# Optimization experiments

Hardware: AMD Instinct MI355X
Metric: run time of the kernel (lower is better)

The kernel has to match this reference:

```python
import jax, jax.numpy as jnp
import numpy as np

N_NODES = 50000
N_EDGES = 1000000
D_IN = 128
HID = 64
N_GRAPHS = 256
NEG_SLOPE = 0.2


def _gatv2_layer(x, src, dst, Wl, Wr, att, b, n_nodes):
    # lin_l applied to source nodes, lin_r to target nodes (PyG GATv2Conv, heads=1)
    xl = x @ Wl.T  # [N, C]
    xr = x @ Wr.T  # [N, C]
    e = jax.nn.leaky_relu(xl[src] + xr[dst], NEG_SLOPE)  # [E, C]
    logits = e @ att  # [E]
    # segment softmax over destination node
    m = jax.ops.segment_max(logits, dst, num_segments=n_nodes)
    ex = jnp.exp(logits - m[dst])
    den = jax.ops.segment_sum(ex, dst, num_segments=n_nodes)
    alpha = ex / den[dst]  # [E]
    out = jax.ops.segment_sum(alpha[:, None] * xl[src], dst, num_segments=n_nodes)
    return out + b


def setup_inputs() -> dict:
    key = jax.random.key(0)
    ks = jax.random.split(key, 32)
    x = jax.random.normal(ks[0], (N_NODES, D_IN), dtype=jnp.float32)
    edge_index = jax.random.randint(ks[1], (2, N_EDGES), 0, N_NODES, dtype=jnp.int64)
    batch = jnp.sort(jax.random.randint(ks[2], (N_NODES,), 0, N_GRAPHS, dtype=jnp.int64))
    inp = {"x": x, "edge_index": edge_index, "batch": batch}
    dims = [D_IN, HID, HID]  # input dim per layer
    kidx = 3
    for i, din in enumerate(dims):
        inp[f"Wl{i}"] = jax.random.normal(ks[kidx], (HID, din), dtype=jnp.float32) * 0.1; kidx += 1
        inp[f"Wr{i}"] = jax.random.normal(ks[kidx], (HID, din), dtype=jnp.float32) * 0.1; kidx += 1
        inp[f"att{i}"] = jax.random.normal(ks[kidx], (HID,), dtype=jnp.float32) * 0.1; kidx += 1
        inp[f"b{i}"] = jnp.zeros((HID,), dtype=jnp.float32)
        inp[f"Rw{i}"] = jax.random.normal(ks[kidx], (HID, din), dtype=jnp.float32) * 0.1; kidx += 1
        inp[f"Rb{i}"] = jnp.zeros((HID,), dtype=jnp.float32)
    inp["Wf"] = jax.random.normal(ks[kidx], (1, HID), dtype=jnp.float32) * 0.1
    inp["bf"] = jnp.zeros((1,), dtype=jnp.float32)
    return inp


def reference(x, edge_index, batch, Wl0, Wr0, att0, b0, Rw0, Rb0,
              Wl1, Wr1, att1, b1, Rw1, Rb1,
              Wl2, Wr2, att2, b2, Rw2, Rb2, Wf, bf):
    n = x.shape[0]
    # add_self_loops=True (PyG default)
    loops = jnp.arange(n, dtype=edge_index.dtype)
    src = jnp.concatenate([edge_index[0], loops])
    dst = jnp.concatenate([edge_index[1], loops])
    layers = [(Wl0, Wr0, att0, b0, Rw0, Rb0),
              (Wl1, Wr1, att1, b1, Rw1, Rb1),
              (Wl2, Wr2, att2, b2, Rw2, Rb2)]
    for i, (Wl, Wr, att, b, Rw, Rb) in enumerate(layers):
        h = _gatv2_layer(x, src, dst, Wl, Wr, att, b, n) + (x @ Rw.T + Rb)  # res=True
        # norm=None -> Identity; dropout inactive at inference
        x = jax.nn.relu(h) if i < len(layers) - 1 else h
    # global_mean_pool
    sums = jax.ops.segment_sum(x, batch, num_segments=N_GRAPHS)
    cnt = jax.ops.segment_sum(jnp.ones((n,), x.dtype), batch, num_segments=N_GRAPHS)
    pooled = sums / jnp.maximum(cnt, 1.0)[:, None]
    return pooled @ Wf.T + bf
```

## Files before the change

### kernel.cpp

```cpp
#include <hip/hip_runtime.h>


#define NN 50000
#define NE 1000000
#define HID 64
#define DIN0 128
#define NG 256
#define NEG 0.2f

#define SCHUNK 1024
#define SNB ((NN + SCHUNK - 1) / SCHUNK)

typedef float f32x4 __attribute__((ext_vector_type(4)));
typedef short s8v __attribute__((ext_vector_type(8)));
typedef short s4v __attribute__((ext_vector_type(4)));
typedef __bf16 bf16x8 __attribute__((ext_vector_type(8)));
typedef _Float16 h2v __attribute__((ext_vector_type(2)));
typedef unsigned u32x2 __attribute__((ext_vector_type(2)));
typedef unsigned short u16;

__device__ __forceinline__ unsigned short f2bf(float f) {
    unsigned u = __float_as_uint(f);
    u = u + 0x7fffu + ((u >> 16) & 1u);
    return (unsigned short)(u >> 16);
}
__device__ __forceinline__ float bf2f(unsigned short v) {
    return __uint_as_float(((unsigned)v) << 16);
}
__device__ __forceinline__ short split_hi(float x) {
    return (short)f2bf(x);
}
__device__ __forceinline__ short split_lo(float x, short hi) {
    return (short)f2bf(x - bf2f((unsigned short)hi));
}
__device__ __forceinline__ h2v u2h(unsigned u) { return __builtin_bit_cast(h2v, u); }
__device__ __forceinline__ unsigned h2u(h2v h) { return __builtin_bit_cast(unsigned, h); }
__device__ __forceinline__ h2v pklo(unsigned a, unsigned b) {
    return u2h(__builtin_amdgcn_perm(b, a, 0x05040100u));
}
__device__ __forceinline__ h2v pkhi(unsigned a, unsigned b) {
    return u2h(__builtin_amdgcn_perm(b, a, 0x07060302u));
}
template <int CTRL>
__device__ __forceinline__ float dpp_mv(float v) {
    return __int_as_float(
        __builtin_amdgcn_update_dpp(0, __float_as_int(v), CTRL, 0xF, 0xF, true));
}
template <int OFF>
__device__ __forceinline__ float swz(float v) {
    return __int_as_float(__builtin_amdgcn_ds_swizzle(__float_as_int(v), OFF));
}
__device__ __forceinline__ float red32_add(float v) {
    unsigned u = __float_as_uint(v);
    u32x2 r = __builtin_amdgcn_permlane32_swap(u, u, false, false);
    return __uint_as_float(r[0]) + __uint_as_float(r[1]);
}
__device__ __forceinline__ float red32_max(float v) {
    unsigned u = __float_as_uint(v);
    u32x2 r = __builtin_amdgcn_permlane32_swap(u, u, false, false);
    return fmaxf(__uint_as_float(r[0]), __uint_as_float(r[1]));
}
__device__ __forceinline__ float octet_sum(float v) {
    v += dpp_mv<0xB1>(v);
    v += dpp_mv<0x4E>(v);
    v += swz<0x101F>(v);
    return v;
}
__device__ __forceinline__ float esum(float v) {
    v += dpp_mv<0x128>(v);
    v += swz<0x401F>(v);
    return red32_add(v);
}
__device__ __forceinline__ float emax(float v) {
    v = fmaxf(v, dpp_mv<0x128>(v));
    v = fmaxf(v, swz<0x401F>(v));
    return red32_max(v);
}

__global__ __launch_bounds__(256) void k_prep(
        const float* __restrict__ Wl0, const float* __restrict__ Wr0, const float* __restrict__ Rw0,
        const float* __restrict__ Wl1, const float* __restrict__ Wr1, const float* __restrict__ Rw1,
        const float* __restrict__ Wl2, const float* __restrict__ Wr2, const float* __restrict__ Rw2,
        const float* __restrict__ att0, const float* __restrict__ att1, const float* __restrict__ att2,
        short* __restrict__ Ws0, short* __restrict__ Ws1, short* __restrict__ Ws2,
        _Float16* __restrict__ attp,
        const int* __restrict__ batch,
        int* __restrict__ startg, int* __restrict__ endg,
        int* __restrict__ cnt8) {
    int i = blockIdx.x * 256 + threadIdx.x;
    if (i < 3 * HID) {
        int L = i >> 6, c = i & 63;
        const float* at = (L == 0) ? att0 : (L == 1) ? att1 : att2;
        float a = at[c];
        attp[L * 2 * HID + c] = (_Float16)(0.6f * a);
        attp[L * 2 * HID + HID + c] = (_Float16)(0.4f * a);
    }
    if (i < NN) {
#pragma unroll
        for (int g = 0; g < 8; g++) cnt8[g * NN + i] = 0;
        int g = batch[i];
        if (i == 0) {
            startg[g] = 0;
            for (int g2 = 0; g2 < g; g2++) { startg[g2] = 0; endg[g2] = 0; }
        } else if (batch[i - 1] != g) {
            startg[g] = i;
            for (int g2 = batch[i - 1] + 1; g2 < g; g2++) { startg[g2] = i; endg[g2] = i; }
        }
        if (i == NN - 1) {
            endg[g] = NN;
            for (int g2 = g + 1; g2 < NG; g2++) { startg[g2] = NN; endg[g2] = NN; }
        } else if (batch[i + 1] != g) {
            endg[g] = i + 1;
        }
    }
    const int L0N = 3 * HID * DIN0;
    const int L1N = 3 * HID * HID;
    if (i >= L0N + 2 * L1N) return;
    const float* Wm; short* Ws; int din, local;
    if (i < L0N) {
        local = i; din = DIN0; Ws = Ws0;
        int m = local / (DIN0 * HID);
        Wm = (m == 0) ? Wl0 : (m == 1) ? Wr0 : Rw0;
    } else if (i < L0N + L1N) {
        local = i - L0N; din = HID; Ws = Ws1;
        int m = local / (HID * HID);
        Wm = (m == 0) ? Wl1 : (m == 1) ? Wr1 : Rw1;
    } else {
        local = i - L0N - L1N; din = HID; Ws = Ws2;
        int m = local / (HID * HID);
        Wm = (m == 0) ? Wl2 : (m == 1) ? Wr2 : Rw2;
    }
    int m = local / (din * HID);
    int r = local - m * (din * HID);
    int c = r / din, k = r - c * din;
    float w = Wm[c * din + k];
    short hi = split_hi(w);
    short lo = split_lo(w, hi);
    Ws[(((m * 2 + 0) * HID + c) * din) + k] = hi;
    Ws[(((m * 2 + 1) * HID + c) * din) + k] = lo;
}

__global__ __launch_bounds__(256) void k_hist8(const int* __restrict__ edst,
                                               int* __restrict__ cnt8,
                                               u16* __restrict__ rank) {
    int* mycnt = cnt8 + (blockIdx.x & 7) * NN;
    for (int e = blockIdx.x * 256 + threadIdx.x; e < NE; e += 512 * 256) {
        int r = atomicAdd(&mycnt[edst[e]], 1);
        rank[e] = (u16)r;
    }
}

__global__ __launch_bounds__(256) void k_histscan(int* __restrict__ cnt8,
                                                  int* __restrict__ cnt,
                                                  int* __restrict__ part) {
    __shared__ int ws[4];
    int b = blockIdx.x, t = threadIdx.x;
    int i0 = b * SCHUNK + t * 4;
    int tot = 0;
#pragma unroll
    for (int j = 0; j < 4; j++) {
        int i = i0 + j;
        if (i < NN) {
            int s = 1;
#pragma unroll
            for (int g = 0; g < 8; g++) {
                int v = cnt8[g * NN + i];
                cnt8[g * NN + i] = s;
                s += v;
            }
            cnt[i] = s;
            tot += s;
        }
    }
#pragma unroll
    for (int o = 32; o; o >>= 1) tot += __shfl_xor(tot, o, 64);
    if ((t & 63) == 0) ws[t >> 6] = tot;
    __syncthreads();
    if (t == 0) part[b] = ws[0] + ws[1] + ws[2] + ws[3];
}

__global__ __launch_bounds__(256) void k_scan_emit(const int* __restrict__ cnt,
                                                   const int* __restrict__ part,
                                                   int* __restrict__ off,
                                                   u16* __restrict__ srcs) {
    __shared__ int tsum[256];
    __shared__ int baseSh;
    int b = blockIdx.x, t = threadIdx.x;
    if (t < 64) {
        int v = (t < b && t < SNB) ? part[t] : 0;
#pragma unroll
        for (int o = 32; o; o >>= 1) v += __shfl_xor(v, o, 64);
        if (t == 0) baseSh = v;
    }
    int i0 = b * SCHUNK + t * 4;
    int e[4], p[4];
    int s = 0;
#pragma unroll
    for (int j = 0; j < 4; j++) {
        int i = i0 + j;
        e[j] = (i < NN) ? cnt[i] : 0;
        p[j] = s;
        s += e[j];
    }
    tsum[t] = s;
    __syncthreads();
    for (int d = 1; d < 256; d <<= 1) {
        int v = (t >= d) ? tsum[t - d] : 0;
        __syncthreads();
        tsum[t] += v;
        __syncthreads();
    }
    int base = baseSh + ((t == 0) ? 0 : tsum[t - 1]);
#pragma unroll
    for (int j = 0; j < 4; j++) {
        int i = i0 + j;
        if (i < NN) {
            int v = base + p[j];
            off[i] = v;
            srcs[v] = (u16)i;
            if (i == NN - 1) off[NN] = v + e[j];
        }
    }
}

__global__ __launch_bounds__(256) void k_scatter_rank(
        const int* __restrict__ esrc, const int* __restrict__ edst,
        const int* __restrict__ off, const int* __restrict__ cnt8,
        const u16* __restrict__ rank, u16* __restrict__ srcs) {
    int e = blockIdx.x * 256 + threadIdx.x;
    if (e >= NE) return;
    int d = edst[e];
    int slice = (e >> 8) & 7;
    int pos = off[d] + cnt8[slice * NN + d] + (int)rank[e];
    srcs[pos] = (u16)esrc[e];
}

template <int DIN, bool RELU>
__global__ __launch_bounds__(256, 3) void k_gemm(
        const float* __restrict__ xin, const short* __restrict__ Ws,
        const float* __restrict__ bvec, const float* __restrict__ rb,
        _Float16* __restrict__ xl16, _Float16* __restrict__ xr16, float* __restrict__ acc) {
    constexpr int LROW = 40;
    __shared__ short lds[20480];
    short* xhi = lds;
    short* xlo = lds + 2560;

    const int tid = threadIdx.x;
    const int w = tid >> 6;
    const int lane = tid & 63;
    const int col = lane & 15;
    const int quad = lane >> 4;
    const int nb0 = blockIdx.x * 64;

    f32x4 d[3][4];
#pragma unroll
    for (int m = 0; m < 3; m++)
#pragma unroll
        for (int ct = 0; ct < 4; ct++) d[m][ct] = (f32x4){0.f, 0.f, 0.f, 0.f};

    for (int c0 = 0; c0 < DIN; c0 += 32) {
        if (c0) __syncthreads();
        for (int u = tid; u < 512; u += 256) {
            int row = u >> 3, kq = u & 7;
            int n = nb0 + row;
            float4 v = make_float4(0.f, 0.f, 0.f, 0.f);
            if (n < NN) {
                v = *(const float4*)&xin[(size_t)n * DIN + c0 + 4 * kq];
                if (RELU) {
                    v.x = fmaxf(v.x, 0.f); v.y = fmaxf(v.y, 0.f);
                    v.z = fmaxf(v.z, 0.f); v.w = fmaxf(v.w, 0.f);
                }
            }
            s4v h, l;
            short h0 = split_hi(v.x), l0 = split_lo(v.x, h0);
            short h1 = split_hi(v.y), l1 = split_lo(v.y, h1);
            short h2 = split_hi(v.z), l2 = split_lo(v.z, h2);
            short h3 = split_hi(v.w), l3 = split_lo(v.w, h3);
            h[0] = h0; h[1] = h1; h[2] = h2; h[3] = h3;
            l[0] = l0; l[1] = l1; l[2] = l2; l[3] = l3;
            *(s4v*)&xhi[row * LROW + 4 * kq] = h;
            *(s4v*)&xlo[row * LROW + 4 * kq] = l;
        }
        for (int u = tid; u < 1536; u += 256) {
            int mp = u >> 8;
            int r = u & 255;
            int c = r >> 2, q = r & 3;
            s8v v = *(const s8v*)&Ws[((mp * HID + c) * DIN) + c0 + 8 * q];
            *(s8v*)&lds[5120 + mp * 2560 + c * LROW + 8 * q] = v;
        }
        __syncthreads();

        bf16x8 a_h = __builtin_bit_cast(bf16x8,
            *(const s8v*)&xhi[(w * 16 + col) * LROW + quad * 8]);
        bf16x8 a_l = __builtin_bit_cast(bf16x8,
            *(const s8v*)&xlo[(w * 16 + col) * LROW + quad * 8]);

#pragma unroll
        for (int m = 0; m < 3; m++) {
#pragma unroll
            for (int ct = 0; ct < 4; ct++) {
                bf16x8 b_h = __builtin_bit_cast(bf16x8,
                    *(const s8v*)&lds[5120 + (m * 2 + 0) * 2560 + (ct * 16 + col) * LROW + quad * 8]);
                bf16x8 b_l = __builtin_bit_cast(bf16x8,
                    *(const s8v*)&lds[5120 + (m * 2 + 1) * 2560 + (ct * 16 + col) * LROW + quad * 8]);
                d[m][ct] = __builtin_amdgcn_mfma_f32_16x16x32_bf16(a_h, b_h, d[m][ct], 0, 0, 0);
                d[m][ct] = __builtin_amdgcn_mfma_f32_16x16x32_bf16(a_h, b_l, d[m][ct], 0, 0, 0);
                d[m][ct] = __builtin_amdgcn_mfma_f32_16x16x32_bf16(a_l, b_h, d[m][ct], 0, 0, 0);
            }
        }
    }

#pragma unroll
    for (int r = 0; r < 4; r++) {
        int n = nb0 + w * 16 + quad * 4 + r;
        if (n >= NN) continue;
        size_t base = (size_t)n * HID;
#pragma unroll
        for (int ct = 0; ct < 4; ct++) {
            int c = ct * 16 + col;
            xl16[base + c] = (_Float16)d[0][ct][r];
            xr16[base + c] = (_Float16)d[1][ct][r];
            acc[base + c] = d[2][ct][r] + bvec[c] + rb[c];
        }
    }
}

__global__ __launch_bounds__(256) void k_attn_dst(
        const int* __restrict__ off, const u16* __restrict__ srcs,
        const _Float16* __restrict__ xl16, const _Float16* __restrict__ xr16,
        const _Float16* __restrict__ attL, float* __restrict__ acc) {
    const int lane = threadIdx.x & 63;
    const int d = blockIdx.x * 4 + (threadIdx.x >> 6);
    if (d >= NN) return;
    const int e = lane >> 3;
    const int cg = lane & 7;

    const int lo = off[d], deg = off[d + 1] - lo;

    uint4 X = *(const uint4*)&xr16[(size_t)d * HID + 8 * cg];
    uint4 A6 = *(const uint4*)&attL[8 * cg];
    uint4 A4 = *(const uint4*)&attL[HID + 8 * cg];
    h2v xh0 = u2h(X.x), xh1 = u2h(X.y), xh2 = u2h(X.z), xh3 = u2h(X.w);
    h2v a60 = u2h(A6.x), a61 = u2h(A6.y), a62 = u2h(A6.z), a63 = u2h(A6.w);
    h2v a40 = u2h(A4.x), a41 = u2h(A4.y), a42 = u2h(A4.z), a43 = u2h(A4.w);

#define EDGE_DOT(S, U, PS)                                                     \
    {                                                                          \
        U = *(const uint4*)&xl16[(size_t)(S) * HID + 8 * cg];                  \
        h2v _v; unsigned _a; float _q0, _q1;                                   \
        _v = u2h(U.x) + xh0; _a = h2u(_v) & 0x7FFF7FFFu;                       \
        _q0 = __builtin_amdgcn_fdot2(a60, _v, 0.f, false);                     \
        _q1 = __builtin_amdgcn_fdot2(a40, u2h(_a), 0.f, false);                \
        _v = u2h(U.y) + xh1; _a = h2u(_v) & 0x7FFF7FFFu;                       \
        _q0 = __builtin_amdgcn_fdot2(a61, _v, _q0, false);                     \
        _q1 = __builtin_amdgcn_fdot2(a41, u2h(_a), _q1, false);                \
        _v = u2h(U.z) + xh2; _a = h2u(_v) & 0x7FFF7FFFu;                       \
        _q0 = __builtin_amdgcn_fdot2(a62, _v, _q0, false);                     \
        _q1 = __builtin_amdgcn_fdot2(a42, u2h(_a), _q1, false);                \
        _v = u2h(U.w) + xh3; _a = h2u(_v) & 0x7FFF7FFFu;                       \
        _q0 = __builtin_amdgcn_fdot2(a63, _v, _q0, false);                     \
        _q1 = __builtin_amdgcn_fdot2(a43, u2h(_a), _q1, false);                \
        PS = _q0 + _q1;                                                        \
    }

    float m = -INFINITY, l = 0.f;
    float4 oA = make_float4(0.f, 0.f, 0.f, 0.f);
    float4 oB = make_float4(0.f, 0.f, 0.f, 0.f);

    for (int base = 0; base < deg; base += 32) {
        const int rem = deg - base;
        int s0 = (int)srcs[lo + min(base + e, deg - 1)];
        int s1 = (int)srcs[lo + min(base + 8 + e, deg - 1)];
        int s2 = (int)srcs[lo + min(base + 16 + e, deg - 1)];
        int s3 = (int)srcs[lo + min(base + 24 + e, deg - 1)];

        uint4 U0, U1, U2, U3;
        float ps0, ps1, ps2, ps3;
        float t0, t1, t2 = -INFINITY, t3 = -INFINITY;
        EDGE_DOT(s0, U0, ps0);
        EDGE_DOT(s1, U1, ps1);
        t0 = octet_sum(ps0);
        t1 = octet_sum(ps1);
        if (base + e >= deg) t0 = -INFINITY;
        if (base + 8 + e >= deg) t1 = -INFINITY;

        const bool do2 = rem > 16;
        if (do2) {
            EDGE_DOT(s2, U2, ps2);
            t2 = octet_sum(ps2);
            if (base + 16 + e >= deg) t2 = -INFINITY;
            if (rem > 24) {
                EDGE_DOT(s3, U3, ps3);
                t3 = octet_sum(ps3);
                if (base + 24 + e >= deg) t3 = -INFINITY;
            } else {
                U3 = U0;
            }
        }

        float cm = emax(fmaxf(fmaxf(t0, t1), fmaxf(t2, t3)));
        if (cm > m) {
            float corr = __expf(m - cm);
            m = cm;
            l *= corr;
            oA.x *= corr; oA.y *= corr; oA.z *= corr; oA.w *= corr;
            oB.x *= corr; oB.y *= corr; oB.z *= corr; oB.w *= corr;
        }
        float p0 = __expf(t0 - m);
        float p1 = __expf(t1 - m);
        l += p0 + p1;
        h2v p01 = {(_Float16)p0, (_Float16)p1};
        oA.x = __builtin_amdgcn_fdot2(p01, pklo(U0.x, U1.x), oA.x, false);
        oA.y = __builtin_amdgcn_fdot2(p01, pkhi(U0.x, U1.x), oA.y, false);
        oA.z = __builtin_amdgcn_fdot2(p01, pklo(U0.y, U1.y), oA.z, false);
        oA.w = __builtin_amdgcn_fdot2(p01, pkhi(U0.y, U1.y), oA.w, false);
        oB.x = __builtin_amdgcn_fdot2(p01, pklo(U0.z, U1.z), oB.x, false);
        oB.y = __builtin_amdgcn_fdot2(p01, pkhi(U0.z, U1.z), oB.y, false);
        oB.z = __builtin_amdgcn_fdot2(p01, pklo(U0.w, U1.w), oB.z, false);
        oB.w = __builtin_amdgcn_fdot2(p01, pkhi(U0.w, U1.w), oB.w, false);
        if (do2) {
            float p2 = __expf(t2 - m);
            float p3 = __expf(t3 - m);
            l += p2 + p3;
            h2v p23 = {(_Float16)p2, (_Float16)p3};
            oA.x = __builtin_amdgcn_fdot2(p23, pklo(U2.x, U3.x), oA.x, false);
            oA.y = __builtin_amdgcn_fdot2(p23, pkhi(U2.x, U3.x), oA.y, false);
            oA.z = __builtin_amdgcn_fdot2(p23, pklo(U2.y, U3.y), oA.z, false);
            oA.w = __builtin_amdgcn_fdot2(p23, pkhi(U2.y, U3.y), oA.w, false);
            oB.x = __builtin_amdgcn_fdot2(p23, pklo(U2.z, U3.z), oB.x, false);
            oB.y = __builtin_amdgcn_fdot2(p23, pkhi(U2.z, U3.z), oB.y, false);
            oB.z = __builtin_amdgcn_fdot2(p23, pklo(U2.w, U3.w), oB.z, false);
            oB.w = __builtin_amdgcn_fdot2(p23, pkhi(U2.w, U3.w), oB.w, false);
        }
    }
#undef EDGE_DOT

    l    = esum(l);
    oA.x = esum(oA.x); oA.y = esum(oA.y);
    oA.z = esum(oA.z); oA.w = esum(oA.w);
    oB.x = esum(oB.x); oB.y = esum(oB.y);
    oB.z = esum(oB.z); oB.w = esum(oB.w);

    if (e == 0) {
        float inv = 1.f / l;
        float4* a4 = (float4*)&acc[(size_t)d * HID + 8 * cg];
        float4 c0 = a4[0], c1 = a4[1];
        c0.x += oA.x * inv; c0.y += oA.y * inv;
        c0.z += oA.z * inv; c0.w += oA.w * inv;
        c1.x += oB.x * inv; c1.y += oB.y * inv;
        c1.z += oB.z * inv; c1.w += oB.w * inv;
        a4[0] = c0; a4[1] = c1;
    }
}

__global__ __launch_bounds__(512) void k_pool_final(
        const float* __restrict__ acc,
        const int* __restrict__ startg, const int* __restrict__ endg,
        const float* __restrict__ Wf, const float* __restrict__ bf_,
        float* __restrict__ out) {
    __shared__ float red[8][HID];
    const int g = blockIdx.x;
    const int c = threadIdx.x & 63;
    const int j = threadIdx.x >> 6;
    const int s = startg[g], epos = endg[g];

    float sum = 0.f;
    for (int n = s + j; n < epos; n += 8)
        sum += acc[(size_t)n * HID + c];
    red[j][c] = sum;
    __syncthreads();

    if (threadIdx.x < HID) {
        float tot = 0.f;
#pragma unroll
        for (int w = 0; w < 8; w++) tot += red[w][c];
        float cntf = (float)(epos - s);
        float v = tot / fmaxf(cntf, 1.f) * Wf[c];
#pragma unroll
        for (int o = 32; o; o >>= 1) v += __shfl_xor(v, o, 64);
        if (c == 0) out[g] = v + bf_[0];
    }
}

extern "C" void kernel_launch(void* const* d_in, const int* in_sizes, int n_in,
                              void* d_out, int out_size, void* d_ws, size_t ws_size,
                              hipStream_t stream) {
    const float* x   = (const float*)d_in[0];
    const int* eidx  = (const int*)d_in[1];
    const int* batch = (const int*)d_in[2];
    const int* esrc = eidx;
    const int* edst = eidx + NE;
    const float* Wf  = (const float*)d_in[21];
    const float* bfb = (const float*)d_in[22];

    float* wsf = (float*)d_ws;
    const size_t NN64 = (size_t)NN * HID;
    _Float16* xl16 = (_Float16*)wsf;
    _Float16* xr16 = (_Float16*)(wsf + NN64);
    float* acc0   = wsf + 2 * NN64;
    float* acc1   = acc0 + NN64;
    short* Ws0    = (short*)(acc1 + NN64);
    short* Ws1    = Ws0 + 2 * 3 * HID * DIN0;
    short* Ws2    = Ws1 + 2 * 3 * HID * HID;
    int*   ccnt   = (int*)(Ws2 + 2 * 3 * HID * HID);
    int*   startg = ccnt + NN;
    int*   endg   = startg + NG;
    int*   off    = endg + NG;
    int*   part   = off + NN + 1;
    int*   partSc = part + SNB;
    int*   cnt8   = partSc + SNB;
    u16*   rank   = (u16*)(cnt8 + 8 * NN);
    u16*   srcs   = rank + NE;
    _Float16* attp = (_Float16*)(srcs + NE + NN);

    k_prep<<<(NN + 255) / 256, 256, 0, stream>>>(
        (const float*)d_in[3], (const float*)d_in[4], (const float*)d_in[7],
        (const float*)d_in[9], (const float*)d_in[10], (const float*)d_in[13],
        (const float*)d_in[15], (const float*)d_in[16], (const float*)d_in[19],
        (const float*)d_in[5], (const float*)d_in[11], (const float*)d_in[17],
        Ws0, Ws1, Ws2, attp, batch, startg, endg, cnt8);

    k_hist8<<<512, 256, 0, stream>>>(edst, cnt8, rank);
    k_histscan<<<SNB, 256, 0, stream>>>(cnt8, ccnt, part);
    k_scan_emit<<<SNB, 256, 0, stream>>>(ccnt, part, off, srcs);
    k_scatter_rank<<<(NE + 255) / 256, 256, 0, stream>>>(esrc, edst, off, cnt8, rank, srcs);

    const short* Wss[3] = {Ws0, Ws1, Ws2};
    float* accs[4] = {acc0, acc0, acc1, acc0};
    const int gemm_grid = (NN + 63) / 64;
    for (int L = 0; L < 3; L++) {
        const float* b   = (const float*)d_in[3 + L * 6 + 3];
        const float* Rb  = (const float*)d_in[3 + L * 6 + 5];
        float* accOut = accs[L + 1];

        if (L == 0)
            k_gemm<DIN0, false><<<gemm_grid, 256, 0, stream>>>(
                x, Wss[0], b, Rb, xl16, xr16, accOut);
        else
            k_gemm<HID, true><<<gemm_grid, 256, 0, stream>>>(
                accs[L], Wss[L], b, Rb, xl16, xr16, accOut);

        k_attn_dst<<<(NN + 3) / 4, 256, 0, stream>>>(
            off, srcs, xl16, xr16, attp + L * 2 * HID, accOut);
    }

    k_pool_final<<<NG, 512, 0, stream>>>(accs[3], startg, endg, Wf, bfb, (float*)d_out);
}
```

Baseline: 325.7 us.

## Process two destination nodes per wavefront with batched gathers before logits

Each wavefront now handles two destination nodes. All source-feature gathers for the first 32 edges of both nodes are issued up front, before any logit math, to expose more memory-level parallelism on the irregular gathers. Nodes with more than 32 incoming edges fall back to the original online-softmax loop. This raises register pressure and may lower occupancy. The grid becomes NN/8 blocks with no bounds check, which relies on NN being divisible by 8.

```diff
diff --git a/kernel.cpp b/kernel.cpp
--- a/kernel.cpp
+++ b/kernel.cpp
@@ -330,125 +330,190 @@
         const _Float16* __restrict__ xl16, const _Float16* __restrict__ xr16,
         const _Float16* __restrict__ attL, float* __restrict__ acc) {
     const int lane = threadIdx.x & 63;
-    const int d = blockIdx.x * 4 + (threadIdx.x >> 6);
-    if (d >= NN) return;
+    const int d0 = blockIdx.x * 8 + (threadIdx.x >> 6) * 2;
+    const int d1 = d0 + 1;
     const int e = lane >> 3;
     const int cg = lane & 7;
 
-    const int lo = off[d], deg = off[d + 1] - lo;
-
-    uint4 X = *(const uint4*)&xr16[(size_t)d * HID + 8 * cg];
+    const int lo0 = off[d0], deg0 = off[d0 + 1] - lo0;
+    const int lo1 = off[d1], deg1 = off[d1 + 1] - lo1;
+
+    uint4 X0 = *(const uint4*)&xr16[(size_t)d0 * HID + 8 * cg];
+    uint4 X1 = *(const uint4*)&xr16[(size_t)d1 * HID + 8 * cg];
     uint4 A6 = *(const uint4*)&attL[8 * cg];
     uint4 A4 = *(const uint4*)&attL[HID + 8 * cg];
-    h2v xh0 = u2h(X.x), xh1 = u2h(X.y), xh2 = u2h(X.z), xh3 = u2h(X.w);
+    h2v x00 = u2h(X0.x), x01 = u2h(X0.y), x02 = u2h(X0.z), x03 = u2h(X0.w);
+    h2v x10 = u2h(X1.x), x11 = u2h(X1.y), x12 = u2h(X1.z), x13 = u2h(X1.w);
     h2v a60 = u2h(A6.x), a61 = u2h(A6.y), a62 = u2h(A6.z), a63 = u2h(A6.w);
     h2v a40 = u2h(A4.x), a41 = u2h(A4.y), a42 = u2h(A4.z), a43 = u2h(A4.w);
 
-#define EDGE_DOT(S, U, PS)                                                     \
+#define GATHER(S) (*(const uint4*)&xl16[(size_t)(S) * HID + 8 * cg])
+#define LOGIT(U, XH0, XH1, XH2, XH3, T)                                        \
     {                                                                          \
-        U = *(const uint4*)&xl16[(size_t)(S) * HID + 8 * cg];                  \
         h2v _v; unsigned _a; float _q0, _q1;                                   \
-        _v = u2h(U.x) + xh0; _a = h2u(_v) & 0x7FFF7FFFu;                       \
+        _v = u2h(U.x) + XH0; _a = h2u(_v) & 0x7FFF7FFFu;                       \
         _q0 = __builtin_amdgcn_fdot2(a60, _v, 0.f, false);                     \
         _q1 = __builtin_amdgcn_fdot2(a40, u2h(_a), 0.f, false);                \
-        _v = u2h(U.y) + xh1; _a = h2u(_v) & 0x7FFF7FFFu;                       \
+        _v = u2h(U.y) + XH1; _a = h2u(_v) & 0x7FFF7FFFu;                       \
         _q0 = __builtin_amdgcn_fdot2(a61, _v, _q0, false);                     \
         _q1 = __builtin_amdgcn_fdot2(a41, u2h(_a), _q1, false);                \
-        _v = u2h(U.z) + xh2; _a = h2u(_v) & 0x7FFF7FFFu;                       \
+        _v = u2h(U.z) + XH2; _a = h2u(_v) & 0x7FFF7FFFu;                       \
         _q0 = __builtin_amdgcn_fdot2(a62, _v, _q0, false);                     \
         _q1 = __builtin_amdgcn_fdot2(a42, u2h(_a), _q1, false);                \
-        _v = u2h(U.w) + xh3; _a = h2u(_v) & 0x7FFF7FFFu;                       \
+        _v = u2h(U.w) + XH3; _a = h2u(_v) & 0x7FFF7FFFu;                       \
         _q0 = __builtin_amdgcn_fdot2(a63, _v, _q0, false);                     \
         _q1 = __builtin_amdgcn_fdot2(a43, u2h(_a), _q1, false);                \
-        PS = _q0 + _q1;                                                        \
-    }
-
-    float m = -INFINITY, l = 0.f;
-    float4 oA = make_float4(0.f, 0.f, 0.f, 0.f);
-    float4 oB = make_float4(0.f, 0.f, 0.f, 0.f);
-
-    for (int base = 0; base < deg; base += 32) {
-        const int rem = deg - base;
-        int s0 = (int)srcs[lo + min(base + e, deg - 1)];
-        int s1 = (int)srcs[lo + min(base + 8 + e, deg - 1)];
-        int s2 = (int)srcs[lo + min(base + 16 + e, deg - 1)];
-        int s3 = (int)srcs[lo + min(base + 24 + e, deg - 1)];
-
-        uint4 U0, U1, U2, U3;
-        float ps0, ps1, ps2, ps3;
-        float t0, t1, t2 = -INFINITY, t3 = -INFINITY;
-        EDGE_DOT(s0, U0, ps0);
-        EDGE_DOT(s1, U1, ps1);
-        t0 = octet_sum(ps0);
-        t1 = octet_sum(ps1);
-        if (base + e >= deg) t0 = -INFINITY;
-        if (base + 8 + e >= deg) t1 = -INFINITY;
-
-        const bool do2 = rem > 16;
-        if (do2) {
-            EDGE_DOT(s2, U2, ps2);
-            t2 = octet_sum(ps2);
-            if (base + 16 + e >= deg) t2 = -INFINITY;
-            if (rem > 24) {
-                EDGE_DOT(s3, U3, ps3);
-                t3 = octet_sum(ps3);
-                if (base + 24 + e >= deg) t3 = -INFINITY;
-            } else {
-                U3 = U0;
-            }
-        }
-
-        float cm = emax(fmaxf(fmaxf(t0, t1), fmaxf(t2, t3)));
-        if (cm > m) {
-            float corr = __expf(m - cm);
-            m = cm;
-            l *= corr;
-            oA.x *= corr; oA.y *= corr; oA.z *= corr; oA.w *= corr;
-            oB.x *= corr; oB.y *= corr; oB.z *= corr; oB.w *= corr;
-        }
-        float p0 = __expf(t0 - m);
-        float p1 = __expf(t1 - m);
-        l += p0 + p1;
-        h2v p01 = {(_Float16)p0, (_Float16)p1};
-        oA.x = __builtin_amdgcn_fdot2(p01, pklo(U0.x, U1.x), oA.x, false);
-        oA.y = __builtin_amdgcn_fdot2(p01, pkhi(U0.x, U1.x), oA.y, false);
-        oA.z = __builtin_amdgcn_fdot2(p01, pklo(U0.y, U1.y), oA.z, false);
-        oA.w = __builtin_amdgcn_fdot2(p01, pkhi(U0.y, U1.y), oA.w, false);
-        oB.x = __builtin_amdgcn_fdot2(p01, pklo(U0.z, U1.z), oB.x, false);
-        oB.y = __builtin_amdgcn_fdot2(p01, pkhi(U0.z, U1.z), oB.y, false);
-        oB.z = __builtin_amdgcn_fdot2(p01, pklo(U0.w, U1.w), oB.z, false);
-        oB.w = __builtin_amdgcn_fdot2(p01, pkhi(U0.w, U1.w), oB.w, false);
-        if (do2) {
-            float p2 = __expf(t2 - m);
-            float p3 = __expf(t3 - m);
-            l += p2 + p3;
-            h2v p23 = {(_Float16)p2, (_Float16)p3};
-            oA.x = __builtin_amdgcn_fdot2(p23, pklo(U2.x, U3.x), oA.x, false);
-            oA.y = __builtin_amdgcn_fdot2(p23, pkhi(U2.x, U3.x), oA.y, false);
-            oA.z = __builtin_amdgcn_fdot2(p23, pklo(U2.y, U3.y), oA.z, false);
-            oA.w = __builtin_amdgcn_fdot2(p23, pkhi(U2.y, U3.y), oA.w, false);
-            oB.x = __builtin_amdgcn_fdot2(p23, pklo(U2.z, U3.z), oB.x, false);
-            oB.y = __builtin_amdgcn_fdot2(p23, pkhi(U2.z, U3.z), oB.y, false);
-            oB.z = __builtin_amdgcn_fdot2(p23, pklo(U2.w, U3.w), oB.z, false);
-            oB.w = __builtin_amdgcn_fdot2(p23, pkhi(U2.w, U3.w), oB.w, false);
-        }
-    }
-#undef EDGE_DOT
-
-    l    = esum(l);
-    oA.x = esum(oA.x); oA.y = esum(oA.y);
-    oA.z = esum(oA.z); oA.w = esum(oA.w);
-    oB.x = esum(oB.x); oB.y = esum(oB.y);
-    oB.z = esum(oB.z); oB.w = esum(oB.w);
-
-    if (e == 0) {
-        float inv = 1.f / l;
-        float4* a4 = (float4*)&acc[(size_t)d * HID + 8 * cg];
+        T = octet_sum(_q0 + _q1);                                              \
+    }
+#define PVACC(P, Ua, Ub, OA, OB)                                               \
+    OA.x = __builtin_amdgcn_fdot2(P, pklo(Ua.x, Ub.x), OA.x, false);           \
+    OA.y = __builtin_amdgcn_fdot2(P, pkhi(Ua.x, Ub.x), OA.y, false);           \
+    OA.z = __builtin_amdgcn_fdot2(P, pklo(Ua.y, Ub.y), OA.z, false);           \
+    OA.w = __builtin_amdgcn_fdot2(P, pkhi(Ua.y, Ub.y), OA.w, false);           \
+    OB.x = __builtin_amdgcn_fdot2(P, pklo(Ua.z, Ub.z), OB.x, false);           \
+    OB.y = __builtin_amdgcn_fdot2(P, pkhi(Ua.z, Ub.z), OB.y, false);           \
+    OB.z = __builtin_amdgcn_fdot2(P, pklo(Ua.w, Ub.w), OB.z, false);           \
+    OB.w = __builtin_amdgcn_fdot2(P, pkhi(Ua.w, Ub.w), OB.w, false);
+
+    int s00 = (int)srcs[lo0 + min(e, deg0 - 1)];
+    int s01 = (int)srcs[lo0 + min(8 + e, deg0 - 1)];
+    int s02 = (int)srcs[lo0 + min(16 + e, deg0 - 1)];
+    int s03 = (int)srcs[lo0 + min(24 + e, deg0 - 1)];
+    int s10 = (int)srcs[lo1 + min(e, deg1 - 1)];
+    int s11 = (int)srcs[lo1 + min(8 + e, deg1 - 1)];
+    int s12 = (int)srcs[lo1 + min(16 + e, deg1 - 1)];
+    int s13 = (int)srcs[lo1 + min(24 + e, deg1 - 1)];
+    const int mdeg = max(deg0, deg1);
+
+    uint4 U00 = GATHER(s00), U01 = GATHER(s01);
+    uint4 U10 = GATHER(s10), U11 = GATHER(s11);
+    uint4 U02, U03, U12, U13;
+    float t00, t01, t02 = -INFINITY, t03 = -INFINITY;
+    float t10, t11, t12 = -INFINITY, t13 = -INFINITY;
+    const bool do2 = mdeg > 16, do3 = mdeg > 24;
+    if (do2) {
+        U02 = GATHER(s02); U12 = GATHER(s12);
+        if (do3) { U03 = GATHER(s03); U13 = GATHER(s13); }
+        else     { U03 = U00; U13 = U10; }
+    }
+    LOGIT(U00, x00, x01, x02, x03, t00);
+    LOGIT(U01, x00, x01, x02, x03, t01);
+    LOGIT(U10, x10, x11, x12, x13, t10);
+    LOGIT(U11, x10, x11, x12, x13, t11);
+    if (e >= deg0) t00 = -INFINITY;
+    if (8 + e >= deg0) t01 = -INFINITY;
+    if (e >= deg1) t10 = -INFINITY;
+    if (8 + e >= deg1) t11 = -INFINITY;
+    if (do2) {
+        LOGIT(U02, x00, x01, x02, x03, t02);
+        LOGIT(U12, x10, x11, x12, x13, t12);
+        if (16 + e >= deg0) t02 = -INFINITY;
+        if (16 + e >= deg1) t12 = -INFINITY;
+        if (do3) {
+            LOGIT(U03, x00, x01, x02, x03, t03);
+            LOGIT(U13, x10, x11, x12, x13, t13);
+            if (24 + e >= deg0) t03 = -INFINITY;
+            if (24 + e >= deg1) t13 = -INFINITY;
+        }
+    }
+
+    float m0 = emax(fmaxf(fmaxf(t00, t01), fmaxf(t02, t03)));
+    float m1 = emax(fmaxf(fmaxf(t10, t11), fmaxf(t12, t13)));
+
+    float p00 = __expf(t00 - m0), p01 = __expf(t01 - m0);
+    float p10 = __expf(t10 - m1), p11 = __expf(t11 - m1);
+    float l0 = p00 + p01, l1 = p10 + p11;
+    float4 oA0 = make_float4(0.f, 0.f, 0.f, 0.f), oB0 = oA0;
+    float4 oA1 = oA0, oB1 = oA0;
+    {
+        h2v pa = {(_Float16)p00, (_Float16)p01};
+        h2v pb = {(_Float16)p10, (_Float16)p11};
+        PVACC(pa, U00, U01, oA0, oB0)
+        PVACC(pb, U10, U11, oA1, oB1)
+    }
+    if (do2) {
+        float p02 = __expf(t02 - m0), p03 = __expf(t03 - m0);
+        float p12 = __expf(t12 - m1), p13 = __expf(t13 - m1);
+        l0 += p02 + p03; l1 += p12 + p13;
+        h2v pa = {(_Float16)p02, (_Float16)p03};
+        h2v pb = {(_Float16)p12, (_Float16)p13};
+        PVACC(pa, U02, U03, oA0, oB0)
+        PVACC(pb, U12, U13, oA1, oB1)
+    }
+
+#define GENLOOP(LO, DEG, XH0, XH1, XH2, XH3, M, L, OA, OB)                     \
+    for (int base = 32; base < DEG; base += 32) {                              \
+        const int rem = DEG - base;                                            \
+        int s0 = (int)srcs[LO + min(base + e, DEG - 1)];                       \
+        int s1 = (int)srcs[LO + min(base + 8 + e, DEG - 1)];                   \
+        int s2 = (int)srcs[LO + min(base + 16 + e, DEG - 1)];                  \
+        int s3 = (int)srcs[LO + min(base + 24 + e, DEG - 1)];                  \
+        uint4 V0 = GATHER(s0), V1 = GATHER(s1), V2, V3;                        \
+        float u0, u1, u2 = -INFINITY, u3 = -INFINITY;                          \
+        LOGIT(V0, XH0, XH1, XH2, XH3, u0);                                     \
+        LOGIT(V1, XH0, XH1, XH2, XH3, u1);                                     \
+        if (base + e >= DEG) u0 = -INFINITY;                                   \
+        if (base + 8 + e >= DEG) u1 = -INFINITY;                               \
+        const bool c2 = rem > 16;                                              \
+        if (c2) {                                                              \
+            V2 = GATHER(s2);                                                   \
+            LOGIT(V2, XH0, XH1, XH2, XH3, u2);                                 \
+            if (base + 16 + e >= DEG) u2 = -INFINITY;                          \
+            if (rem > 24) {                                                    \
+                V3 = GATHER(s3);                                               \
+                LOGIT(V3, XH0, XH1, XH2, XH3, u3);                             \
+                if (base + 24 + e >= DEG) u3 = -INFINITY;                      \
+            } else { V3 = V0; }                                                \
+        }                                                                      \
+        float cm = emax(fmaxf(fmaxf(u0, u1), fmaxf(u2, u3)));                  \
+        if (cm > M) {                                                          \
+            float corr = __expf(M - cm);                                       \
+            M = cm;                                                            \
+            L *= corr;                                                         \
+            OA.x *= corr; OA.y *= corr; OA.z *= corr; OA.w *= corr;            \
+            OB.x *= corr; OB.y *= corr; OB.z *= corr; OB.w *= corr;            \
+        }                                                                      \
+        float q0 = __expf(u0 - M), q1 = __expf(u1 - M);                        \
+        L += q0 + q1;                                                          \
+        h2v qp = {(_Float16)q0, (_Float16)q1};                                 \
+        PVACC(qp, V0, V1, OA, OB)                                              \
+        if (c2) {                                                              \
+            float q2 = __expf(u2 - M), q3 = __expf(u3 - M);                    \
+            L += q2 + q3;                                                      \
+            h2v qq = {(_Float16)q2, (_Float16)q3};                             \
+            PVACC(qq, V2, V3, OA, OB)                                          \
+        }                                                                      \
+    }
+
+    if (deg0 > 32) { GENLOOP(lo0, deg0, x00, x01, x02, x03, m0, l0, oA0, oB0) }
+    if (deg1 > 32) { GENLOOP(lo1, deg1, x10, x11, x12, x13, m1, l1, oA1, oB1) }
+#undef GENLOOP
+#undef GATHER
+#undef LOGIT
+#undef PVACC
+
+    l0    = esum(l0);    l1    = esum(l1);
+    oA0.x = esum(oA0.x); oA1.x = esum(oA1.x);
+    oA0.y = esum(oA0.y); oA1.y = esum(oA1.y);
+    oA0.z = esum(oA0.z); oA1.z = esum(oA1.z);
+    oA0.w = esum(oA0.w); oA1.w = esum(oA1.w);
+    oB0.x = esum(oB0.x); oB1.x = esum(oB1.x);
+    oB0.y = esum(oB0.y); oB1.y = esum(oB1.y);
+    oB0.z = esum(oB0.z); oB1.z = esum(oB1.z);
+    oB0.w = esum(oB0.w); oB1.w = esum(oB1.w);
+
+    if (e < 2) {
+        const bool s = (e == 1);
+        int dd = s ? d1 : d0;
+        float inv = 1.f / (s ? l1 : l0);
+        float4 wA = s ? oA1 : oA0;
+        float4 wB = s ? oB1 : oB0;
+        float4* a4 = (float4*)&acc[(size_t)dd * HID + 8 * cg];
         float4 c0 = a4[0], c1 = a4[1];
-        c0.x += oA.x * inv; c0.y += oA.y * inv;
-        c0.z += oA.z * inv; c0.w += oA.w * inv;
-        c1.x += oB.x * inv; c1.y += oB.y * inv;
-        c1.z += oB.z * inv; c1.w += oB.w * inv;
+        c0.x += wA.x * inv; c0.y += wA.y * inv;
+        c0.z += wA.z * inv; c0.w += wA.w * inv;
+        c1.x += wB.x * inv; c1.y += wB.y * inv;
+        c1.z += wB.z * inv; c1.w += wB.w * inv;
         a4[0] = c0; a4[1] = c1;
     }
 }
@@ -540,7 +605,7 @@
             k_gemm<HID, true><<<gemm_grid, 256, 0, stream>>>(
                 accs[L], Wss[L], b, Rb, xl16, xr16, accOut);
 
-        k_attn_dst<<<(NN + 3) / 4, 256, 0, stream>>>(
+        k_attn_dst<<<NN / 8, 256, 0, stream>>>(
             off, srcs, xl16, xr16, attp + L * 2 * HID, accOut);
     }
 
```

Result: faster. 310.2 us (-4.8%).
